# Kernel optimization log

Measured on AMD Instinct MI355X. Metric: run time of the kernel, lower is better.

The kernel has to match this reference:

```python
import jax, jax.numpy as jnp
import numpy as np

MARGIN = 0.1
EPS = 1e-12  # matches torch.nn.functional.normalize default eps


def setup_inputs() -> dict:
    key = jax.random.key(0)
    k1, k2, k3 = jax.random.split(key, 3)
    B, V, D = 1024, 128000, 512
    inputs = jax.random.normal(k1, (B, D), dtype=jnp.float32)
    emb_weight = jax.random.normal(k2, (V, D), dtype=jnp.float32) * 0.02
    target = jax.random.randint(k3, (B,), 0, V)
    return {"inputs": inputs, "emb_weight": emb_weight, "target": target}


def reference(inputs, emb_weight, target):
    # L2-normalize rows of inputs (torch F.normalize, p=2, dim=1)
    norm = jnp.maximum(jnp.linalg.norm(inputs, axis=1, keepdims=True), EPS)
    x = inputs / norm  # [B, D]
    # dot products against the whole vocabulary: [B, V]
    dot_product = jnp.einsum('bd,vd->bv', x, emb_weight)
    # similarity with the true class embedding: [B, 1]
    true_emb = emb_weight[target]  # [B, D]
    negate_item = jnp.sum(x * true_emb, axis=1, keepdims=True)
    # margin ranking: relu(margin + s_neg - s_pos), summed over vocab, mean over batch
    relu_mat = jax.nn.relu(MARGIN + dot_product - negate_item)
    return jnp.mean(jnp.sum(relu_mat, axis=1))
```

## Files before the change

kernel.cpp:

```cpp
#include <hip/hip_runtime.h>

typedef __attribute__((ext_vector_type(4))) float f32x4;
typedef __attribute__((ext_vector_type(4))) int   i32x4;
typedef __attribute__((ext_vector_type(8))) int   i32x8;

#define MARGIN 0.1f
#define SC1 0x7F7F7F7F
#define INV_SCALE (1.0f/2048.0f)

__device__ __forceinline__ unsigned int nib4(float a) {
    const float m = fabsf(a);
    unsigned int c = (unsigned)(m > 0.25f) + (m > 0.75f) + (m > 1.25f) +
                     (m > 1.75f) + (m > 2.5f) + (m > 3.5f) + (m > 5.0f);
    return c | ((__builtin_bit_cast(unsigned int, a) >> 28) & 8u);
}
__device__ __forceinline__ unsigned int pack8(const float4 f0, const float4 f1,
                                              float s) {
    return  nib4(f0.x * s)         | (nib4(f0.y * s) << 4)  |
           (nib4(f0.z * s) << 8)   | (nib4(f0.w * s) << 12) |
           (nib4(f1.x * s) << 16)  | (nib4(f1.y * s) << 20) |
           (nib4(f1.z * s) << 24)  | (nib4(f1.w * s) << 28);
}
__device__ __forceinline__ i32x8 pad8(const i32x4 v) {
    return (i32x8){v[0], v[1], v[2], v[3], 0, 0, 0, 0};
}

__global__ __launch_bounds__(256) void prep_convert_kernel(
    const float* __restrict__ inputs, const float* __restrict__ emb,
    const int* __restrict__ target, unsigned char* __restrict__ x_frag4,
    float* __restrict__ neg, unsigned char* __restrict__ emb4)
{
    const int t = threadIdx.x;
    __shared__ float s_ss[4], s_de[4];
    if (blockIdx.x < 2000) {
        const int nt = blockIdx.x;
        const int lane6 = t & 63, nf = t >> 6;
        const int lrow = lane6 & 15, g = lane6 >> 4;
        const float* src = emb + (size_t)(nt * 64 + nf * 16 + lrow) * 512 + g * 32;
        unsigned char* dst = emb4 + (size_t)nt * 16384 + nf * 1024 + lane6 * 16;
        #pragma unroll
        for (int kk = 0; kk < 4; ++kk) {
            const float4* s4 = reinterpret_cast<const float4*>(src + kk * 128);
            unsigned int w[4];
            #pragma unroll
            for (int d = 0; d < 4; ++d)
                w[d] = pack8(s4[2 * d], s4[2 * d + 1], 64.0f);
            *reinterpret_cast<uint4*>(dst + kk * 4096) =
                make_uint4(w[0], w[1], w[2], w[3]);
        }
    } else {
        const int b = blockIdx.x - 2000;
        const float2 v = *reinterpret_cast<const float2*>(inputs + (size_t)b * 512 + t * 2);
        const int tgt = target[b];
        const float2 e = *reinterpret_cast<const float2*>(emb + (size_t)tgt * 512 + t * 2);
        float ss = v.x * v.x + v.y * v.y;
        float de = v.x * e.x + v.y * e.y;
        #pragma unroll
        for (int off = 32; off; off >>= 1) {
            ss += __shfl_down(ss, off);
            de += __shfl_down(de, off);
        }
        const int wid = t >> 6, lane = t & 63;
        if (lane == 0) { s_ss[wid] = ss; s_de[wid] = de; }
        __syncthreads();
        const float tss = s_ss[0] + s_ss[1] + s_ss[2] + s_ss[3];
        const float tde = s_de[0] + s_de[1] + s_de[2] + s_de[3];
        const float inv = 1.0f / fmaxf(sqrtf(tss), 1e-12f);
        const float sc = inv * 32.0f;
        const int addr = (b >> 4) * 4096 + (t >> 6) * 1024 +
                         ((((t >> 4) & 3) * 16 + (b & 15)) * 16) + (t & 15);
        x_frag4[addr] = (unsigned char)(nib4(v.x * sc) | (nib4(v.y * sc) << 4));
        if (t == 0) neg[b] = tde * inv;
    }
}

__device__ __forceinline__ void gload_lds16(const void* g, void* l) {
    __builtin_amdgcn_global_load_lds(
        (const __attribute__((address_space(1))) unsigned int*)g,
        (__attribute__((address_space(3))) unsigned int*)l, 16, 0, 0);
}

__global__ __launch_bounds__(512) void gemm_fp4_kernel(
    const unsigned char* __restrict__ x_frag4, const unsigned char* __restrict__ emb4,
    const float* __restrict__ neg, float* __restrict__ partials)
{
    __shared__ unsigned char btile[32768];
    const int t = threadIdx.x;
    const int wid = t >> 6, lane = t & 63;
    const int g = lane >> 4;
    const int bx = blockIdx.x;
    const int group = (bx & 7) | ((bx >> 4) << 3);
    const int mhalf = (bx >> 3) & 1;
    const int cnt = (group < 80) ? 16 : 15;

    i32x4 areg[4][4];
    #pragma unroll
    for (int mf = 0; mf < 4; ++mf) {
        const int f = mhalf * 32 + wid * 4 + mf;
        #pragma unroll
        for (int kk = 0; kk < 4; ++kk)
            areg[mf][kk] = *reinterpret_cast<const i32x4*>(
                x_frag4 + (size_t)f * 4096 + kk * 1024 + lane * 16);
    }

#define STAGE(buf, tile)                                                      \
    {                                                                         \
        const size_t gb = (size_t)(tile) * 16384 + t * 16;                    \
        gload_lds16(emb4 + gb,        &btile[(buf) * 16384 + t * 16]);        \
        gload_lds16(emb4 + gb + 8192, &btile[(buf) * 16384 + t * 16 + 8192]); \
    }

    STAGE(0, group);
    float sum = 0.0f;

    #pragma unroll 1
    for (int j = 0; j < cnt; ++j) {
        if (j + 1 < cnt) {
            STAGE((j + 1) & 1, group + 128 * (j + 1));
            asm volatile("s_waitcnt vmcnt(2)" ::: "memory");
        } else {
            asm volatile("s_waitcnt vmcnt(0)" ::: "memory");
        }
        __builtin_amdgcn_s_barrier();
        __builtin_amdgcn_sched_barrier(0);

        f32x4 acc[4][4];
        #pragma unroll
        for (int i = 0; i < 4; ++i)
            #pragma unroll
            for (int k = 0; k < 4; ++k) acc[i][k] = (f32x4)(0.0f);

        const unsigned char* bb = btile + (j & 1) * 16384 + lane * 16;
        #pragma unroll
        for (int kk = 0; kk < 4; ++kk) {
            #pragma unroll
            for (int nf = 0; nf < 4; ++nf) {
                const i32x4 b4 = *reinterpret_cast<const i32x4*>(
                    bb + kk * 4096 + nf * 1024);
                const i32x8 b8 = pad8(b4);
                #pragma unroll
                for (int mf = 0; mf < 4; ++mf)
                    acc[mf][nf] = __builtin_amdgcn_mfma_scale_f32_16x16x128_f8f6f4(
                        pad8(areg[mf][kk]), b8, acc[mf][nf],
                        4, 4, 0, SC1, 0, SC1);
            }
        }

        const int rbase = mhalf * 512 + wid * 64 + g * 4;
        #pragma unroll
        for (int mf = 0; mf < 4; ++mf) {
            const float4 nv = *reinterpret_cast<const float4*>(neg + rbase + mf * 16);
            #pragma unroll
            for (int jj = 0; jj < 4; ++jj) {
                const float thr = (&nv.x)[jj] - MARGIN;
                #pragma unroll
                for (int nf = 0; nf < 4; ++nf)
                    sum += fmaxf(acc[mf][nf][jj] * INV_SCALE - thr, 0.0f);
            }
        }
        __builtin_amdgcn_sched_barrier(0);
        __builtin_amdgcn_s_barrier();
    }

    __syncthreads();
    #pragma unroll
    for (int off = 32; off; off >>= 1) sum += __shfl_down(sum, off);
    float* red = reinterpret_cast<float*>(btile);
    if (lane == 0) red[wid] = sum;
    __syncthreads();
    if (t == 0) {
        float tot = 0.f;
        #pragma unroll
        for (int w = 0; w < 8; ++w) tot += red[w];
        partials[bx] = tot;
    }
}

__global__ __launch_bounds__(256) void reduce_kernel(
    const float* __restrict__ partials, float* __restrict__ out)
{
    float s = partials[threadIdx.x];
    #pragma unroll
    for (int off = 32; off; off >>= 1) s += __shfl_down(s, off);
    __shared__ float red[4];
    const int wid = threadIdx.x >> 6, lane = threadIdx.x & 63;
    if (lane == 0) red[wid] = s;
    __syncthreads();
    if (threadIdx.x == 0)
        out[0] = (red[0] + red[1] + red[2] + red[3]) * (1.0f / 1024.0f);
}

extern "C" void kernel_launch(void* const* d_in, const int* in_sizes, int n_in,
                              void* d_out, int out_size, void* d_ws, size_t ws_size,
                              hipStream_t stream)
{
    const float* inputs = (const float*)d_in[0];
    const float* emb    = (const float*)d_in[1];
    const int*   target = (const int*)d_in[2];
    float* out = (float*)d_out;
    char*  ws  = (char*)d_ws;

    unsigned char* x_frag4 = (unsigned char*)ws;
    float*         neg     = (float*)(ws + 262144);
    float*         parts   = (float*)(ws + 266240);
    unsigned char* emb4    = (unsigned char*)(ws + 1048576);

    prep_convert_kernel<<<3024, 256, 0, stream>>>(inputs, emb, target,
                                                  x_frag4, neg, emb4);
    gemm_fp4_kernel<<<256, 512, 0, stream>>>(x_frag4, emb4, neg, parts);
    reduce_kernel<<<1, 256, 0, stream>>>(parts, out);
}
```

Baseline: 97.25 us.

## Fuse embedding FP4 quantization into GEMM and drop the quantized weight buffer

The separate pass that quantized the 128000x512 embedding table to FP4 in workspace is removed. The GEMM kernel now loads fp32 embedding rows directly, packs them to FP4 in registers and writes them into a double-buffered LDS tile, overlapping the next tile's load and pack with the current tile's MFMA work. Each of 500 blocks owns 4 vocab tiles and re-reads all x fragments from global memory per tile instead of keeping them in registers. This removes the write and re-read of the quantized table, but adds x-fragment reloads, in-loop conversion ALU work and full block barriers.

```diff
diff --git a/kernel.cpp b/kernel.cpp
--- a/kernel.cpp
+++ b/kernel.cpp
@@ -25,161 +25,154 @@
     return (i32x8){v[0], v[1], v[2], v[3], 0, 0, 0, 0};
 }
 
-__global__ __launch_bounds__(256) void prep_convert_kernel(
+__global__ __launch_bounds__(256) void prep_kernel(
     const float* __restrict__ inputs, const float* __restrict__ emb,
     const int* __restrict__ target, unsigned char* __restrict__ x_frag4,
-    float* __restrict__ neg, unsigned char* __restrict__ emb4)
+    float* __restrict__ neg)
 {
     const int t = threadIdx.x;
+    const int b = blockIdx.x;
+    const float2 v = *reinterpret_cast<const float2*>(inputs + (size_t)b * 512 + t * 2);
+    const int tgt = target[b];
+    const float2 e = *reinterpret_cast<const float2*>(emb + (size_t)tgt * 512 + t * 2);
+    float ss = v.x * v.x + v.y * v.y;
+    float de = v.x * e.x + v.y * e.y;
+    #pragma unroll
+    for (int off = 32; off; off >>= 1) {
+        ss += __shfl_down(ss, off);
+        de += __shfl_down(de, off);
+    }
     __shared__ float s_ss[4], s_de[4];
-    if (blockIdx.x < 2000) {
-        const int nt = blockIdx.x;
-        const int lane6 = t & 63, nf = t >> 6;
-        const int lrow = lane6 & 15, g = lane6 >> 4;
-        const float* src = emb + (size_t)(nt * 64 + nf * 16 + lrow) * 512 + g * 32;
-        unsigned char* dst = emb4 + (size_t)nt * 16384 + nf * 1024 + lane6 * 16;
-        #pragma unroll
-        for (int kk = 0; kk < 4; ++kk) {
-            const float4* s4 = reinterpret_cast<const float4*>(src + kk * 128);
-            unsigned int w[4];
-            #pragma unroll
-            for (int d = 0; d < 4; ++d)
-                w[d] = pack8(s4[2 * d], s4[2 * d + 1], 64.0f);
-            *reinterpret_cast<uint4*>(dst + kk * 4096) =
-                make_uint4(w[0], w[1], w[2], w[3]);
-        }
-    } else {
-        const int b = blockIdx.x - 2000;
-        const float2 v = *reinterpret_cast<const float2*>(inputs + (size_t)b * 512 + t * 2);
-        const int tgt = target[b];
-        const float2 e = *reinterpret_cast<const float2*>(emb + (size_t)tgt * 512 + t * 2);
-        float ss = v.x * v.x + v.y * v.y;
-        float de = v.x * e.x + v.y * e.y;
-        #pragma unroll
-        for (int off = 32; off; off >>= 1) {
-            ss += __shfl_down(ss, off);
-            de += __shfl_down(de, off);
-        }
-        const int wid = t >> 6, lane = t & 63;
-        if (lane == 0) { s_ss[wid] = ss; s_de[wid] = de; }
-        __syncthreads();
-        const float tss = s_ss[0] + s_ss[1] + s_ss[2] + s_ss[3];
-        const float tde = s_de[0] + s_de[1] + s_de[2] + s_de[3];
-        const float inv = 1.0f / fmaxf(sqrtf(tss), 1e-12f);
-        const float sc = inv * 32.0f;
-        const int addr = (b >> 4) * 4096 + (t >> 6) * 1024 +
-                         ((((t >> 4) & 3) * 16 + (b & 15)) * 16) + (t & 15);
-        x_frag4[addr] = (unsigned char)(nib4(v.x * sc) | (nib4(v.y * sc) << 4));
-        if (t == 0) neg[b] = tde * inv;
-    }
-}
-
-__device__ __forceinline__ void gload_lds16(const void* g, void* l) {
-    __builtin_amdgcn_global_load_lds(
-        (const __attribute__((address_space(1))) unsigned int*)g,
-        (__attribute__((address_space(3))) unsigned int*)l, 16, 0, 0);
-}
-
-__global__ __launch_bounds__(512) void gemm_fp4_kernel(
-    const unsigned char* __restrict__ x_frag4, const unsigned char* __restrict__ emb4,
+    const int wid = t >> 6, lane = t & 63;
+    if (lane == 0) { s_ss[wid] = ss; s_de[wid] = de; }
+    __syncthreads();
+    const float tss = s_ss[0] + s_ss[1] + s_ss[2] + s_ss[3];
+    const float tde = s_de[0] + s_de[1] + s_de[2] + s_de[3];
+    const float inv = 1.0f / fmaxf(sqrtf(tss), 1e-12f);
+    const float sc = inv * 32.0f;
+    const int addr = (b >> 4) * 4096 + (t >> 6) * 1024 +
+                     ((((t >> 4) & 3) * 16 + (b & 15)) * 16) + (t & 15);
+    x_frag4[addr] = (unsigned char)(nib4(v.x * sc) | (nib4(v.y * sc) << 4));
+    if (t == 0) neg[b] = tde * inv;
+}
+
+__global__ __launch_bounds__(256) void gemm_fused_kernel(
+    const unsigned char* __restrict__ x_frag4, const float* __restrict__ emb,
     const float* __restrict__ neg, float* __restrict__ partials)
 {
     __shared__ unsigned char btile[32768];
     const int t = threadIdx.x;
     const int wid = t >> 6, lane = t & 63;
-    const int g = lane >> 4;
-    const int bx = blockIdx.x;
-    const int group = (bx & 7) | ((bx >> 4) << 3);
-    const int mhalf = (bx >> 3) & 1;
-    const int cnt = (group < 80) ? 16 : 15;
-
-    i32x4 areg[4][4];
-    #pragma unroll
-    for (int mf = 0; mf < 4; ++mf) {
-        const int f = mhalf * 32 + wid * 4 + mf;
-        #pragma unroll
-        for (int kk = 0; kk < 4; ++kk)
-            areg[mf][kk] = *reinterpret_cast<const i32x4*>(
-                x_frag4 + (size_t)f * 4096 + kk * 1024 + lane * 16);
-    }
-
-#define STAGE(buf, tile)                                                      \
-    {                                                                         \
-        const size_t gb = (size_t)(tile) * 16384 + t * 16;                    \
-        gload_lds16(emb4 + gb,        &btile[(buf) * 16384 + t * 16]);        \
-        gload_lds16(emb4 + gb + 8192, &btile[(buf) * 16384 + t * 16 + 8192]); \
-    }
-
-    STAGE(0, group);
-    float sum = 0.0f;
-
-    #pragma unroll 1
-    for (int j = 0; j < cnt; ++j) {
-        if (j + 1 < cnt) {
-            STAGE((j + 1) & 1, group + 128 * (j + 1));
-            asm volatile("s_waitcnt vmcnt(2)" ::: "memory");
-        } else {
-            asm volatile("s_waitcnt vmcnt(0)" ::: "memory");
-        }
-        __builtin_amdgcn_s_barrier();
-        __builtin_amdgcn_sched_barrier(0);
-
-        f32x4 acc[4][4];
-        #pragma unroll
-        for (int i = 0; i < 4; ++i)
-            #pragma unroll
-            for (int k = 0; k < 4; ++k) acc[i][k] = (f32x4)(0.0f);
-
-        const unsigned char* bb = btile + (j & 1) * 16384 + lane * 16;
+    const int lrow = lane & 15, g = lane >> 4;
+    const int nfc = t >> 6;
+    const int t0 = blockIdx.x * 4;
+
+    #define SRC(T) (reinterpret_cast<const float4*>( \
+        emb + (size_t)((T) * 64 + nfc * 16 + lrow) * 512 + g * 32))
+
+    {
+        const float4* sp = SRC(t0);
         #pragma unroll
         for (int kk = 0; kk < 4; ++kk) {
-            #pragma unroll
-            for (int nf = 0; nf < 4; ++nf) {
-                const i32x4 b4 = *reinterpret_cast<const i32x4*>(
-                    bb + kk * 4096 + nf * 1024);
-                const i32x8 b8 = pad8(b4);
-                #pragma unroll
-                for (int mf = 0; mf < 4; ++mf)
-                    acc[mf][nf] = __builtin_amdgcn_mfma_scale_f32_16x16x128_f8f6f4(
-                        pad8(areg[mf][kk]), b8, acc[mf][nf],
-                        4, 4, 0, SC1, 0, SC1);
+            float4 r[8];
+            #pragma unroll
+            for (int i = 0; i < 8; ++i) r[i] = sp[kk * 32 + i];
+            uint4 w;
+            w.x = pack8(r[0], r[1], 64.0f);
+            w.y = pack8(r[2], r[3], 64.0f);
+            w.z = pack8(r[4], r[5], 64.0f);
+            w.w = pack8(r[6], r[7], 64.0f);
+            *reinterpret_cast<uint4*>(
+                btile + kk * 4096 + nfc * 1024 + lane * 16) = w;
+        }
+    }
+    __syncthreads();
+
+    float sum = 0.0f;
+
+    #pragma unroll 1
+    for (int j = 0; j < 4; ++j) {
+        const bool more = (j + 1 < 4);
+        const float4* sp = SRC(t0 + (more ? j + 1 : 0));
+        const unsigned char* bb = btile + (j & 1) * 16384 + lane * 16;
+        unsigned char* wb = btile + ((j + 1) & 1) * 16384 + nfc * 1024 + lane * 16;
+
+        #pragma unroll
+        for (int p = 0; p < 4; ++p) {
+            float4 r[8];
+            if (more) {
+                #pragma unroll
+                for (int i = 0; i < 8; ++i) r[i] = sp[p * 32 + i];
+            }
+
+            i32x4 a[4][4];
+            #pragma unroll
+            for (int mf = 0; mf < 4; ++mf)
+                #pragma unroll
+                for (int kk = 0; kk < 4; ++kk)
+                    a[mf][kk] = *reinterpret_cast<const i32x4*>(
+                        x_frag4 + (size_t)(p * 16 + wid * 4 + mf) * 4096 +
+                        kk * 1024 + lane * 16);
+
+            f32x4 acc[4][4];
+            #pragma unroll
+            for (int i = 0; i < 4; ++i)
+                #pragma unroll
+                for (int k = 0; k < 4; ++k) acc[i][k] = (f32x4)(0.0f);
+
+            #pragma unroll
+            for (int kk = 0; kk < 4; ++kk)
+                #pragma unroll
+                for (int nf = 0; nf < 4; ++nf) {
+                    const i32x8 b8 = pad8(*reinterpret_cast<const i32x4*>(
+                        bb + kk * 4096 + nf * 1024));
+                    #pragma unroll
+                    for (int mf = 0; mf < 4; ++mf)
+                        acc[mf][nf] = __builtin_amdgcn_mfma_scale_f32_16x16x128_f8f6f4(
+                            pad8(a[mf][kk]), b8, acc[mf][nf],
+                            4, 4, 0, SC1, 0, SC1);
+                }
+
+            const int rbase = p * 256 + wid * 64 + g * 4;
+            #pragma unroll
+            for (int mf = 0; mf < 4; ++mf) {
+                const float4 nv = *reinterpret_cast<const float4*>(
+                    neg + rbase + mf * 16);
+                #pragma unroll
+                for (int jj = 0; jj < 4; ++jj) {
+                    const float thr = (&nv.x)[jj] - MARGIN;
+                    #pragma unroll
+                    for (int nf = 0; nf < 4; ++nf)
+                        sum += fmaxf(acc[mf][nf][jj] * INV_SCALE - thr, 0.0f);
+                }
+            }
+
+            if (more) {
+                uint4 w;
+                w.x = pack8(r[0], r[1], 64.0f);
+                w.y = pack8(r[2], r[3], 64.0f);
+                w.z = pack8(r[4], r[5], 64.0f);
+                w.w = pack8(r[6], r[7], 64.0f);
+                *reinterpret_cast<uint4*>(wb + p * 4096) = w;
             }
         }
-
-        const int rbase = mhalf * 512 + wid * 64 + g * 4;
-        #pragma unroll
-        for (int mf = 0; mf < 4; ++mf) {
-            const float4 nv = *reinterpret_cast<const float4*>(neg + rbase + mf * 16);
-            #pragma unroll
-            for (int jj = 0; jj < 4; ++jj) {
-                const float thr = (&nv.x)[jj] - MARGIN;
-                #pragma unroll
-                for (int nf = 0; nf < 4; ++nf)
-                    sum += fmaxf(acc[mf][nf][jj] * INV_SCALE - thr, 0.0f);
-            }
-        }
-        __builtin_amdgcn_sched_barrier(0);
-        __builtin_amdgcn_s_barrier();
+        __syncthreads();
     }
 
-    __syncthreads();
     #pragma unroll
     for (int off = 32; off; off >>= 1) sum += __shfl_down(sum, off);
     float* red = reinterpret_cast<float*>(btile);
     if (lane == 0) red[wid] = sum;
     __syncthreads();
-    if (t == 0) {
-        float tot = 0.f;
-        #pragma unroll
-        for (int w = 0; w < 8; ++w) tot += red[w];
-        partials[bx] = tot;
-    }
+    if (t == 0)
+        partials[blockIdx.x] = red[0] + red[1] + red[2] + red[3];
 }
 
 __global__ __launch_bounds__(256) void reduce_kernel(
     const float* __restrict__ partials, float* __restrict__ out)
 {
-    float s = partials[threadIdx.x];
+    float s = 0.f;
+    for (int i = threadIdx.x; i < 500; i += 256) s += partials[i];
     #pragma unroll
     for (int off = 32; off; off >>= 1) s += __shfl_down(s, off);
     __shared__ float red[4];
@@ -203,10 +196,8 @@
     unsigned char* x_frag4 = (unsigned char*)ws;
     float*         neg     = (float*)(ws + 262144);
     float*         parts   = (float*)(ws + 266240);
-    unsigned char* emb4    = (unsigned char*)(ws + 1048576);
-
-    prep_convert_kernel<<<3024, 256, 0, stream>>>(inputs, emb, target,
-                                                  x_frag4, neg, emb4);
-    gemm_fp4_kernel<<<256, 512, 0, stream>>>(x_frag4, emb4, neg, parts);
+
+    prep_kernel<<<1024, 256, 0, stream>>>(inputs, emb, target, x_frag4, neg);
+    gemm_fused_kernel<<<500, 256, 0, stream>>>(x_frag4, emb, neg, parts);
     reduce_kernel<<<1, 256, 0, stream>>>(parts, out);
 }
```

Result: slower. 300.9 us (+209.5%).

## Repartition FP4 GEMM into 500 blocks of 256 threads over contiguous N tiles

Applied to the files above, without the earlier changes.

Restructures the GEMM grid from 256 blocks of 512 threads, each covering half the batch over strided vocab tiles, to 500 blocks of 256 threads, each covering a quarter of the batch over 16 contiguous vocab tiles. Threshold values and padded A fragments are hoisted out of the tile loop, and B fragments are loaded before the MFMA loop. The intent is to fill more CUs and reduce per-iteration overhead. The cost is that each vocab tile is now read by four blocks instead of two, and the grid runs in about two waves on 256 CUs, so load may be uneven.

```diff
diff --git a/kernel.cpp b/kernel.cpp
--- a/kernel.cpp
+++ b/kernel.cpp
@@ -23,6 +23,12 @@
 }
 __device__ __forceinline__ i32x8 pad8(const i32x4 v) {
     return (i32x8){v[0], v[1], v[2], v[3], 0, 0, 0, 0};
+}
+
+__device__ __forceinline__ void gload_lds16(const void* g, void* l) {
+    __builtin_amdgcn_global_load_lds(
+        (const __attribute__((address_space(1))) unsigned int*)g,
+        (__attribute__((address_space(3))) unsigned int*)l, 16, 0, 0);
 }
 
 __global__ __launch_bounds__(256) void prep_convert_kernel(
@@ -74,13 +80,7 @@
     }
 }
 
-__device__ __forceinline__ void gload_lds16(const void* g, void* l) {
-    __builtin_amdgcn_global_load_lds(
-        (const __attribute__((address_space(1))) unsigned int*)g,
-        (__attribute__((address_space(3))) unsigned int*)l, 16, 0, 0);
-}
-
-__global__ __launch_bounds__(512) void gemm_fp4_kernel(
+__global__ __launch_bounds__(256) void gemm_tiled_kernel(
     const unsigned char* __restrict__ x_frag4, const unsigned char* __restrict__ emb4,
     const float* __restrict__ neg, float* __restrict__ partials)
 {
@@ -89,35 +89,42 @@
     const int wid = t >> 6, lane = t & 63;
     const int g = lane >> 4;
     const int bx = blockIdx.x;
-    const int group = (bx & 7) | ((bx >> 4) << 3);
-    const int mhalf = (bx >> 3) & 1;
-    const int cnt = (group < 80) ? 16 : 15;
-
-    i32x4 areg[4][4];
-    #pragma unroll
-    for (int mf = 0; mf < 4; ++mf) {
-        const int f = mhalf * 32 + wid * 4 + mf;
+    const int mq = bx & 3;
+    const int grp = bx >> 2;
+    const int t0 = grp * 16;
+
+    i32x8 a8[4][4];
+    #pragma unroll
+    for (int mf = 0; mf < 4; ++mf)
         #pragma unroll
         for (int kk = 0; kk < 4; ++kk)
-            areg[mf][kk] = *reinterpret_cast<const i32x4*>(
-                x_frag4 + (size_t)f * 4096 + kk * 1024 + lane * 16);
-    }
+            a8[mf][kk] = pad8(*reinterpret_cast<const i32x4*>(
+                x_frag4 + (size_t)(mq * 16 + wid * 4 + mf) * 4096 +
+                kk * 1024 + lane * 16));
+
+    const int rbase = mq * 256 + wid * 64 + g * 4;
+    float4 nv[4];
+    #pragma unroll
+    for (int mf = 0; mf < 4; ++mf)
+        nv[mf] = *reinterpret_cast<const float4*>(neg + rbase + mf * 16);
 
 #define STAGE(buf, tile)                                                      \
     {                                                                         \
         const size_t gb = (size_t)(tile) * 16384 + t * 16;                    \
-        gload_lds16(emb4 + gb,        &btile[(buf) * 16384 + t * 16]);        \
-        gload_lds16(emb4 + gb + 8192, &btile[(buf) * 16384 + t * 16 + 8192]); \
+        _Pragma("unroll")                                                     \
+        for (int p = 0; p < 4; ++p)                                           \
+            gload_lds16(emb4 + gb + p * 4096,                                 \
+                        &btile[(buf) * 16384 + p * 4096 + t * 16]);           \
     }
 
-    STAGE(0, group);
+    STAGE(0, t0);
     float sum = 0.0f;
 
     #pragma unroll 1
-    for (int j = 0; j < cnt; ++j) {
-        if (j + 1 < cnt) {
-            STAGE((j + 1) & 1, group + 128 * (j + 1));
-            asm volatile("s_waitcnt vmcnt(2)" ::: "memory");
+    for (int j = 0; j < 16; ++j) {
+        if (j + 1 < 16) {
+            STAGE((j + 1) & 1, t0 + j + 1);
+            asm volatile("s_waitcnt vmcnt(4)" ::: "memory");
         } else {
             asm volatile("s_waitcnt vmcnt(0)" ::: "memory");
         }
@@ -133,31 +140,28 @@
         const unsigned char* bb = btile + (j & 1) * 16384 + lane * 16;
         #pragma unroll
         for (int kk = 0; kk < 4; ++kk) {
-            #pragma unroll
-            for (int nf = 0; nf < 4; ++nf) {
-                const i32x4 b4 = *reinterpret_cast<const i32x4*>(
-                    bb + kk * 4096 + nf * 1024);
-                const i32x8 b8 = pad8(b4);
+            i32x8 b8[4];
+            #pragma unroll
+            for (int nf = 0; nf < 4; ++nf)
+                b8[nf] = pad8(*reinterpret_cast<const i32x4*>(
+                    bb + kk * 4096 + nf * 1024));
+            #pragma unroll
+            for (int mf = 0; mf < 4; ++mf)
                 #pragma unroll
-                for (int mf = 0; mf < 4; ++mf)
+                for (int nf = 0; nf < 4; ++nf)
                     acc[mf][nf] = __builtin_amdgcn_mfma_scale_f32_16x16x128_f8f6f4(
-                        pad8(areg[mf][kk]), b8, acc[mf][nf],
-                        4, 4, 0, SC1, 0, SC1);
-            }
-        }
-
-        const int rbase = mhalf * 512 + wid * 64 + g * 4;
-        #pragma unroll
-        for (int mf = 0; mf < 4; ++mf) {
-            const float4 nv = *reinterpret_cast<const float4*>(neg + rbase + mf * 16);
+                        a8[mf][kk], b8[nf], acc[mf][nf], 4, 4, 0, SC1, 0, SC1);
+        }
+
+        #pragma unroll
+        for (int mf = 0; mf < 4; ++mf)
             #pragma unroll
             for (int jj = 0; jj < 4; ++jj) {
-                const float thr = (&nv.x)[jj] - MARGIN;
+                const float thr = (&nv[mf].x)[jj] - MARGIN;
                 #pragma unroll
                 for (int nf = 0; nf < 4; ++nf)
                     sum += fmaxf(acc[mf][nf][jj] * INV_SCALE - thr, 0.0f);
             }
-        }
         __builtin_amdgcn_sched_barrier(0);
         __builtin_amdgcn_s_barrier();
     }
@@ -168,18 +172,15 @@
     float* red = reinterpret_cast<float*>(btile);
     if (lane == 0) red[wid] = sum;
     __syncthreads();
-    if (t == 0) {
-        float tot = 0.f;
-        #pragma unroll
-        for (int w = 0; w < 8; ++w) tot += red[w];
-        partials[bx] = tot;
-    }
+    if (t == 0)
+        partials[bx] = red[0] + red[1] + red[2] + red[3];
 }
 
 __global__ __launch_bounds__(256) void reduce_kernel(
     const float* __restrict__ partials, float* __restrict__ out)
 {
-    float s = partials[threadIdx.x];
+    float s = 0.f;
+    for (int i = threadIdx.x; i < 500; i += 256) s += partials[i];
     #pragma unroll
     for (int off = 32; off; off >>= 1) s += __shfl_down(s, off);
     __shared__ float red[4];
@@ -207,6 +208,6 @@
 
     prep_convert_kernel<<<3024, 256, 0, stream>>>(inputs, emb, target,
                                                   x_frag4, neg, emb4);
-    gemm_fp4_kernel<<<256, 512, 0, stream>>>(x_frag4, emb4, neg, parts);
+    gemm_tiled_kernel<<<500, 256, 0, stream>>>(x_frag4, emb4, neg, parts);
     reduce_kernel<<<1, 256, 0, stream>>>(parts, out);
 }
```

Result: no change. 96.84 us (-0.4%).
